# Optimization experiments

Measured on AMD Instinct MI355X. Metric: run time of the kernel, lower is better.

The kernel has to match this reference:

```python
import jax, jax.numpy as jnp
import numpy as np

MARGIN = 0.2  # init kwarg
_EPS = 1e-12


def _pairwise_dist(x):
    # Euclidean cdist via the Gram trick; safe sqrt so grads stay finite at d=0.
    sq = jnp.sum(x * x, axis=1)
    d2 = sq[:, None] + sq[None, :] - 2.0 * (x @ x.T)
    d2 = jnp.maximum(d2, 0.0)
    safe = jnp.where(d2 > _EPS, d2, _EPS)
    return jnp.where(d2 > _EPS, jnp.sqrt(safe), 0.0)


def setup_inputs() -> dict:
    key = jax.random.key(0)
    k1, k2 = jax.random.split(key)
    B, D = 8192, 128
    embeddings = jax.random.normal(k1, (B, D), dtype=jnp.float32)
    labels = jax.random.randint(k2, (B,), 0, 64)
    return {"embeddings": embeddings, "labels": labels}


def reference(embeddings, labels):
    B = embeddings.shape[0]
    d = _pairwise_dist(embeddings)                      # [B, B]
    eq = labels[None, :] == labels[:, None]             # [B, B] bool (incl. diag)
    pos_mask = eq.astype(d.dtype) - jnp.eye(B, dtype=d.dtype)  # positives, no self
    hardest_positive = jnp.max(d * pos_mask, axis=1)    # [B]
    max_dist = jnp.max(d)
    # push non-negatives (same label, incl. self) out of the min
    hardest_negative = jnp.min(d + max_dist * eq.astype(d.dtype), axis=1)  # [B]
    losses = jax.nn.relu(hardest_positive - hardest_negative + MARGIN)
    return jnp.mean(losses)
```

## Files before the change

kernel.cpp:

```cpp
#include <hip/hip_runtime.h>
#include <hip/hip_bf16.h>


#define BB 8192
#define DD 128
#define MARGIN 0.2f
#define EPS 1e-12f

#define COLS_PER_BLOCK 512
#define ROWS_PER_BLOCK 256
#define STAGE_COLS 64
#define NSTAGES 8
#define STAGE_SHORTS (STAGE_COLS * DD)

typedef __attribute__((ext_vector_type(8))) short short8;
typedef __attribute__((ext_vector_type(16))) float f32x16;

__device__ inline unsigned short f2bf(float f) {
    __hip_bfloat16 h = __float2bfloat16(f);
    unsigned short u;
    __builtin_memcpy(&u, &h, 2);
    return u;
}

__global__ __launch_bounds__(256) void prep_kernel(
    const float* __restrict__ x, const int* __restrict__ lab,
    unsigned short* __restrict__ xb, float2* __restrict__ meta,
    unsigned* __restrict__ hp2, unsigned* __restrict__ mn2,
    unsigned long long* __restrict__ fsum, unsigned* __restrict__ fdone) {
    int t = blockIdx.x * blockDim.x + threadIdx.x;
    int row = t >> 5;
    const float4 v = reinterpret_cast<const float4*>(x)[t];

    union { unsigned short u[4]; uint2 w; } p;
    p.u[0] = f2bf(v.x); p.u[1] = f2bf(v.y);
    p.u[2] = f2bf(v.z); p.u[3] = f2bf(v.w);
    reinterpret_cast<uint2*>(xb)[t] = p.w;

    float s = v.x * v.x + v.y * v.y + v.z * v.z + v.w * v.w;
    #pragma unroll
    for (int m = 16; m >= 1; m >>= 1) s += __shfl_xor(s, m, 64);
    if ((t & 31) == 0) meta[row] = make_float2(s, __int_as_float(lab[row]));

    if (t < BB) { hp2[t] = 0u; mn2[t] = 0x7f800000u; }
    if (t == 0) { *fsum = 0ull; *fdone = 0u; }
}

__global__ __launch_bounds__(512) void triplet_main(
    const unsigned short* __restrict__ xb, const float2* __restrict__ meta,
    unsigned* __restrict__ hp2, unsigned* __restrict__ mn2) {
    const int tid  = threadIdx.x;
    const int wave = tid >> 6;
    const int lane = tid & 63;
    const int l31  = lane & 31;
    const int lh1  = lane >> 5;
    const int rbase = blockIdx.x * ROWS_PER_BLOCK + wave * 32;
    const int cbase = blockIdx.y * COLS_PER_BLOCK;

    __shared__ unsigned short sb[3][STAGE_SHORTS];
    __shared__ float2 smeta[COLS_PER_BLOCK];

    short8 a[8];
    {
        const unsigned short* ar = xb + (size_t)(rbase + l31) * DD + lh1 * 8;
        #pragma unroll
        for (int s = 0; s < 8; ++s)
            a[s] = *reinterpret_cast<const short8*>(ar + s * 16);
    }

    unsigned li4[4];
    float hp[16], mn[16];
    #pragma unroll
    for (int q = 0; q < 4; ++q) {
        unsigned w = 0;
        #pragma unroll
        for (int k = 0; k < 4; ++k) {
            const int rl = 8 * q + 4 * lh1 + k;
            w |= ((unsigned)__float_as_int(meta[rbase + rl].y) & 255u) << (8 * k);
        }
        li4[q] = w;
    }
    #pragma unroll
    for (int r = 0; r < 16; ++r) { hp[r] = -__builtin_inff(); mn[r] = __builtin_inff(); }

    smeta[tid] = meta[cbase + tid];

    auto stage = [&](int g, int buf) {
        const char* src_base = (const char*)(xb + (size_t)(cbase + g * STAGE_COLS) * DD);
        #pragma unroll
        for (int p = 0; p < 2; ++p) {
            const int o   = p * 8192 + tid * 16;
            const int row = o >> 8;
            const int byt = (o & 255) ^ ((row & 15) << 4);
            const char* src = src_base + row * 256 + byt;
            char* dst = (char*)&sb[buf][0] + p * 8192 + wave * 1024;
            __builtin_amdgcn_global_load_lds(
                (const __attribute__((address_space(1))) void*)src,
                (__attribute__((address_space(3))) void*)dst, 16, 0, 0);
        }
    };

    auto compute_group = [&](int st, int gg, int buf) {
        const char* base = (const char*)&sb[buf][0];
        const int jl = gg * 32 + l31;
        const int rowoff = jl * 256;
        const int swz = (jl & 15) << 4;
        f32x16 acc = {};
        short8 b[4];
        #pragma unroll
        for (int s = 0; s < 4; ++s)
            b[s] = *reinterpret_cast<const short8*>(
                base + rowoff + ((s * 32 + lh1 * 16) ^ swz));
        #pragma unroll
        for (int s = 0; s < 4; ++s)
            acc = __builtin_amdgcn_mfma_f32_32x32x16_bf16(a[s], b[s], acc, 0, 0, 0);
        #pragma unroll
        for (int s = 0; s < 4; ++s)
            b[s] = *reinterpret_cast<const short8*>(
                base + rowoff + (((s + 4) * 32 + lh1 * 16) ^ swz));
        #pragma unroll
        for (int s = 0; s < 4; ++s)
            acc = __builtin_amdgcn_mfma_f32_32x32x16_bf16(a[s + 4], b[s], acc, 0, 0, 0);

        const float2 mj = smeta[st * STAGE_COLS + jl];
        const float sqj = mj.x;
        const int   lj  = __float_as_int(mj.y);
        #pragma unroll
        for (int q = 0; q < 4; ++q) {
            const unsigned lw = li4[q];
            #pragma unroll
            for (int k = 0; k < 4; ++k) {
                const int r = q * 4 + k;
                const float d2p = fmaf(acc[r], -2.0f, sqj);
                const bool eq = (int)((lw >> (8 * k)) & 255u) == lj;
                hp[r] = fmaxf(hp[r], eq ? d2p : -__builtin_inff());
                mn[r] = fminf(mn[r], eq ? __builtin_inff() : d2p);
            }
        }
    };

    stage(0, 0);
    stage(1, 1);
    #define PIPE_ITER(ST, PEND)                                            \
        asm volatile("s_waitcnt vmcnt(" #PEND ")" ::: "memory");           \
        __syncthreads();                                                   \
        if ((ST) + 2 < NSTAGES) stage((ST) + 2, ((ST) + 2) % 3);           \
        compute_group((ST), 0, (ST) % 3);                                  \
        compute_group((ST), 1, (ST) % 3);
    PIPE_ITER(0, 2)
    PIPE_ITER(1, 2)
    PIPE_ITER(2, 2)
    PIPE_ITER(3, 2)
    PIPE_ITER(4, 2)
    PIPE_ITER(5, 2)
    PIPE_ITER(6, 2)
    PIPE_ITER(7, 0)
    #undef PIPE_ITER

    #pragma unroll
    for (int r = 0; r < 16; ++r) {
        const int rl = (r & 3) + 8 * (r >> 2) + 4 * lh1;
        const float sqi = meta[rbase + rl].x;
        hp[r] = fmaxf(sqi + hp[r], 0.0f);
        mn[r] = sqi + mn[r];
    }
    #pragma unroll
    for (int m = 1; m < 32; m <<= 1) {
        #pragma unroll
        for (int r = 0; r < 16; ++r) {
            hp[r] = fmaxf(hp[r], __shfl_xor(hp[r], m, 64));
            mn[r] = fminf(mn[r], __shfl_xor(mn[r], m, 64));
        }
    }
    if (l31 == 0) {
        #pragma unroll
        for (int r = 0; r < 16; ++r) {
            const int i = rbase + (r & 3) + 8 * (r >> 2) + 4 * lh1;
            atomicMax(&hp2[i], __float_as_uint(hp[r]));
            atomicMin(&mn2[i], __float_as_uint(mn[r]));
        }
    }
}

__device__ inline float d_of(float d2) {
    return (d2 > EPS) ? sqrtf(d2) : 0.0f;
}

__global__ __launch_bounds__(1024) void finalize_kernel(
    const unsigned* __restrict__ hp2, const unsigned* __restrict__ mn2,
    unsigned long long* __restrict__ fsum, unsigned* __restrict__ fdone,
    float* __restrict__ out) {
    const int i = blockIdx.x * 1024 + threadIdx.x;
    const float hpv = d_of(__uint_as_float(hp2[i]));
    const float mnv = d_of(__uint_as_float(mn2[i]));
    float acc = fmaxf(hpv - mnv + MARGIN, 0.0f);

    #pragma unroll
    for (int m = 1; m < 64; m <<= 1) acc += __shfl_xor(acc, m, 64);
    __shared__ float ws[16];
    const int wave = threadIdx.x >> 6;
    if ((threadIdx.x & 63) == 0) ws[wave] = acc;
    __syncthreads();
    if (threadIdx.x == 0) {
        float s = 0.0f;
        #pragma unroll
        for (int w = 0; w < 16; ++w) s += ws[w];
        atomicAdd(fsum, (unsigned long long)((double)s * 4294967296.0));
        __threadfence();
        const unsigned old = atomicAdd(fdone, 1u);
        if (old == gridDim.x - 1) {
            const unsigned long long total = atomicAdd(fsum, 0ull);
            out[0] = (float)((double)total / 4294967296.0 / (double)BB);
        }
    }
}

extern "C" void kernel_launch(void* const* d_in, const int* in_sizes, int n_in,
                              void* d_out, int out_size, void* d_ws, size_t ws_size,
                              hipStream_t stream) {
    const float* x = (const float*)d_in[0];
    const int* lab = (const int*)d_in[1];
    float* out = (float*)d_out;

    char* ws = (char*)d_ws;
    unsigned short* xb = (unsigned short*)ws;
    float2* meta = (float2*)(ws + (size_t)BB * DD * 2);
    unsigned* hp2 = (unsigned*)(ws + (size_t)BB * DD * 2 + BB * 8);
    unsigned* mn2 = (unsigned*)(ws + (size_t)BB * DD * 2 + BB * 12);
    unsigned long long* fsum = (unsigned long long*)(ws + (size_t)BB * DD * 2 + BB * 16);
    unsigned* fdone = (unsigned*)(ws + (size_t)BB * DD * 2 + BB * 16 + 8);

    prep_kernel<<<(BB * DD / 4) / 256, 256, 0, stream>>>(x, lab, xb, meta, hp2, mn2, fsum, fdone);
    dim3 grid(BB / ROWS_PER_BLOCK, BB / COLS_PER_BLOCK);
    triplet_main<<<grid, 512, 0, stream>>>(xb, meta, hp2, mn2);
    finalize_kernel<<<BB / 1024, 1024, 0, stream>>>(hp2, mn2, fsum, fdone, out);
}
```

Measured before the change: 50.18 us.

## Exploit distance symmetry with upper-triangular tiles and fold norms into MFMA

Exploits the symmetry of the distance matrix by launching only upper-triangular 256x256 tile pairs. Each tile updates both its row reductions and, through per-column cross-lane reductions and atomics, the column reductions, which roughly halves the MFMA work. The squared-norm terms are folded into an extra bf16 MFMA so the epilogue works directly on scaled accumulator values. This adds per-group column atomics and shuffles, and it loses precision because the norms pass through bf16. It also swaps __syncthreads for a raw barrier with a scheduling fence.

```diff
diff --git a/kernel.cpp b/kernel.cpp
--- a/kernel.cpp
+++ b/kernel.cpp
@@ -7,10 +7,11 @@
 #define MARGIN 0.2f
 #define EPS 1e-12f
 
-#define COLS_PER_BLOCK 512
-#define ROWS_PER_BLOCK 256
+#define NBLK 32
+#define TILE 256
+#define NTRI (NBLK * (NBLK + 1) / 2)
 #define STAGE_COLS 64
-#define NSTAGES 8
+#define NSTAGES 4
 #define STAGE_SHORTS (STAGE_COLS * DD)
 
 typedef __attribute__((ext_vector_type(8))) short short8;
@@ -54,11 +55,15 @@
     const int lane = tid & 63;
     const int l31  = lane & 31;
     const int lh1  = lane >> 5;
-    const int rbase = blockIdx.x * ROWS_PER_BLOCK + wave * 32;
-    const int cbase = blockIdx.y * COLS_PER_BLOCK;
+
+    int bi = 0, rem = (int)blockIdx.x;
+    while (rem >= NBLK - bi) { rem -= NBLK - bi; ++bi; }
+    const int bj = bi + rem;
+    const int rbase = bi * TILE + wave * 32;
+    const int cbase = bj * TILE;
 
     __shared__ unsigned short sb[3][STAGE_SHORTS];
-    __shared__ float2 smeta[COLS_PER_BLOCK];
+    __shared__ float2 smeta[TILE];
 
     short8 a[8];
     {
@@ -67,9 +72,13 @@
         for (int s = 0; s < 8; ++s)
             a[s] = *reinterpret_cast<const short8*>(ar + s * 16);
     }
+    short8 a9 = {0, 0, 0, 0, 0, 0, 0, 0};
+    if (lh1 == 0) {
+        a9[0] = (short)f2bf(meta[rbase + l31].x);
+        a9[1] = (short)0x3F80;
+    }
 
     unsigned li4[4];
-    float hp[16], mn[16];
     #pragma unroll
     for (int q = 0; q < 4; ++q) {
         unsigned w = 0;
@@ -80,10 +89,11 @@
         }
         li4[q] = w;
     }
-    #pragma unroll
-    for (int r = 0; r < 16; ++r) { hp[r] = -__builtin_inff(); mn[r] = __builtin_inff(); }
-
-    smeta[tid] = meta[cbase + tid];
+    float hpa[16], mna[16];
+    #pragma unroll
+    for (int r = 0; r < 16; ++r) { hpa[r] = __builtin_inff(); mna[r] = -__builtin_inff(); }
+
+    if (tid < TILE) smeta[tid] = meta[cbase + tid];
 
     auto stage = [&](int g, int buf) {
         const char* src_base = (const char*)(xb + (size_t)(cbase + g * STAGE_COLS) * DD);
@@ -105,7 +115,16 @@
         const int jl = gg * 32 + l31;
         const int rowoff = jl * 256;
         const int swz = (jl & 15) << 4;
+        const float2 mj = smeta[st * STAGE_COLS + jl];
+        const int lj = __float_as_int(mj.y) & 255;
+
+        short8 b9 = {0, 0, 0, 0, 0, 0, 0, 0};
+        if (lh1 == 0) {
+            b9[0] = (short)0xBF00;
+            b9[1] = (short)f2bf(-0.5f * mj.x);
+        }
         f32x16 acc = {};
+        acc = __builtin_amdgcn_mfma_f32_32x32x16_bf16(a9, b9, acc, 0, 0, 0);
         short8 b[4];
         #pragma unroll
         for (int s = 0; s < 4; ++s)
@@ -122,62 +141,60 @@
         for (int s = 0; s < 4; ++s)
             acc = __builtin_amdgcn_mfma_f32_32x32x16_bf16(a[s + 4], b[s], acc, 0, 0, 0);
 
-        const float2 mj = smeta[st * STAGE_COLS + jl];
-        const float sqj = mj.x;
-        const int   lj  = __float_as_int(mj.y);
+        float hpc = __builtin_inff(), mnc = -__builtin_inff();
         #pragma unroll
         for (int q = 0; q < 4; ++q) {
             const unsigned lw = li4[q];
             #pragma unroll
             for (int k = 0; k < 4; ++k) {
                 const int r = q * 4 + k;
-                const float d2p = fmaf(acc[r], -2.0f, sqj);
                 const bool eq = (int)((lw >> (8 * k)) & 255u) == lj;
-                hp[r] = fmaxf(hp[r], eq ? d2p : -__builtin_inff());
-                mn[r] = fminf(mn[r], eq ? __builtin_inff() : d2p);
+                const float sp = eq ? acc[r] : __builtin_inff();
+                const float sn = eq ? -__builtin_inff() : acc[r];
+                hpa[r] = fminf(hpa[r], sp);
+                mna[r] = fmaxf(mna[r], sn);
+                hpc = fminf(hpc, sp);
+                mnc = fmaxf(mnc, sn);
             }
+        }
+        hpc = fminf(hpc, __shfl_xor(hpc, 32, 64));
+        mnc = fmaxf(mnc, __shfl_xor(mnc, 32, 64));
+        if (lh1 == 0) {
+            const int j = cbase + st * STAGE_COLS + jl;
+            atomicMax(&hp2[j], __float_as_uint(fmaxf(hpc * -2.0f, 0.0f)));
+            atomicMin(&mn2[j], __float_as_uint(mnc * -2.0f));
         }
     };
 
     stage(0, 0);
     stage(1, 1);
-    #define PIPE_ITER(ST, PEND)                                            \
-        asm volatile("s_waitcnt vmcnt(" #PEND ")" ::: "memory");           \
-        __syncthreads();                                                   \
-        if ((ST) + 2 < NSTAGES) stage((ST) + 2, ((ST) + 2) % 3);           \
-        compute_group((ST), 0, (ST) % 3);                                  \
+    #define PIPE_ITER(ST, PEND)                                                \
+        asm volatile("s_waitcnt lgkmcnt(0) vmcnt(" #PEND ")" ::: "memory");    \
+        __builtin_amdgcn_s_barrier();                                          \
+        __builtin_amdgcn_sched_barrier(0);                                     \
+        if ((ST) + 2 < NSTAGES) stage((ST) + 2, ((ST) + 2) % 3);               \
+        compute_group((ST), 0, (ST) % 3);                                      \
         compute_group((ST), 1, (ST) % 3);
     PIPE_ITER(0, 2)
     PIPE_ITER(1, 2)
     PIPE_ITER(2, 2)
-    PIPE_ITER(3, 2)
-    PIPE_ITER(4, 2)
-    PIPE_ITER(5, 2)
-    PIPE_ITER(6, 2)
-    PIPE_ITER(7, 0)
+    PIPE_ITER(3, 0)
     #undef PIPE_ITER
 
     #pragma unroll
-    for (int r = 0; r < 16; ++r) {
-        const int rl = (r & 3) + 8 * (r >> 2) + 4 * lh1;
-        const float sqi = meta[rbase + rl].x;
-        hp[r] = fmaxf(sqi + hp[r], 0.0f);
-        mn[r] = sqi + mn[r];
-    }
-    #pragma unroll
     for (int m = 1; m < 32; m <<= 1) {
         #pragma unroll
         for (int r = 0; r < 16; ++r) {
-            hp[r] = fmaxf(hp[r], __shfl_xor(hp[r], m, 64));
-            mn[r] = fminf(mn[r], __shfl_xor(mn[r], m, 64));
+            hpa[r] = fminf(hpa[r], __shfl_xor(hpa[r], m, 64));
+            mna[r] = fmaxf(mna[r], __shfl_xor(mna[r], m, 64));
         }
     }
     if (l31 == 0) {
         #pragma unroll
         for (int r = 0; r < 16; ++r) {
             const int i = rbase + (r & 3) + 8 * (r >> 2) + 4 * lh1;
-            atomicMax(&hp2[i], __float_as_uint(hp[r]));
-            atomicMin(&mn2[i], __float_as_uint(mn[r]));
+            atomicMax(&hp2[i], __float_as_uint(fmaxf(hpa[r] * -2.0f, 0.0f)));
+            atomicMin(&mn2[i], __float_as_uint(mna[r] * -2.0f));
         }
     }
 }
@@ -231,7 +248,6 @@
     unsigned* fdone = (unsigned*)(ws + (size_t)BB * DD * 2 + BB * 16 + 8);
 
     prep_kernel<<<(BB * DD / 4) / 256, 256, 0, stream>>>(x, lab, xb, meta, hp2, mn2, fsum, fdone);
-    dim3 grid(BB / ROWS_PER_BLOCK, BB / COLS_PER_BLOCK);
-    triplet_main<<<grid, 512, 0, stream>>>(xb, meta, hp2, mn2);
+    triplet_main<<<NTRI, 512, 0, stream>>>(xb, meta, hp2, mn2);
     finalize_kernel<<<BB / 1024, 1024, 0, stream>>>(hp2, mn2, fsum, fdone, out);
 }
```

New measurement: 86.87 us. 73.1% more time.

## Switch to 16x16x32 MFMA tiles with smaller row blocks and finer pipeline stages

Applied to the files above, without the earlier changes.

Replaces the 32x32x16 bf16 MFMA tiling with 16x16x32 tiles: each wave now owns 16 rows instead of 32, blocks cover 128 rows, and stages hold 32 columns across 16 pipeline steps. This cuts per-thread register state (4 accumulators and mins/maxes instead of 16) and doubles the grid, aiming for more occupancy and better load balance. The pipeline uses explicit s_barrier plus sched_barrier and tighter waitcnt. In exchange, each column tile is reloaded by twice as many blocks, and there are more barriers per column processed.

```diff
diff --git a/kernel.cpp b/kernel.cpp
--- a/kernel.cpp
+++ b/kernel.cpp
@@ -8,13 +8,13 @@
 #define EPS 1e-12f
 
 #define COLS_PER_BLOCK 512
-#define ROWS_PER_BLOCK 256
-#define STAGE_COLS 64
-#define NSTAGES 8
+#define ROWS_PER_BLOCK 128
+#define STAGE_COLS 32
+#define NSTAGES 16
 #define STAGE_SHORTS (STAGE_COLS * DD)
 
 typedef __attribute__((ext_vector_type(8))) short short8;
-typedef __attribute__((ext_vector_type(16))) float f32x16;
+typedef __attribute__((ext_vector_type(4))) float f32x4;
 
 __device__ inline unsigned short f2bf(float f) {
     __hip_bfloat16 h = __float2bfloat16(f);
@@ -52,130 +52,107 @@
     const int tid  = threadIdx.x;
     const int wave = tid >> 6;
     const int lane = tid & 63;
-    const int l31  = lane & 31;
-    const int lh1  = lane >> 5;
-    const int rbase = blockIdx.x * ROWS_PER_BLOCK + wave * 32;
+    const int l15  = lane & 15;
+    const int lhi  = lane >> 4;
+    const int rbase = blockIdx.x * ROWS_PER_BLOCK + wave * 16;
     const int cbase = blockIdx.y * COLS_PER_BLOCK;
 
     __shared__ unsigned short sb[3][STAGE_SHORTS];
     __shared__ float2 smeta[COLS_PER_BLOCK];
 
-    short8 a[8];
+    short8 a[4];
     {
-        const unsigned short* ar = xb + (size_t)(rbase + l31) * DD + lh1 * 8;
-        #pragma unroll
-        for (int s = 0; s < 8; ++s)
-            a[s] = *reinterpret_cast<const short8*>(ar + s * 16);
-    }
-
-    unsigned li4[4];
-    float hp[16], mn[16];
-    #pragma unroll
-    for (int q = 0; q < 4; ++q) {
-        unsigned w = 0;
-        #pragma unroll
-        for (int k = 0; k < 4; ++k) {
-            const int rl = 8 * q + 4 * lh1 + k;
-            w |= ((unsigned)__float_as_int(meta[rbase + rl].y) & 255u) << (8 * k);
-        }
-        li4[q] = w;
-    }
-    #pragma unroll
-    for (int r = 0; r < 16; ++r) { hp[r] = -__builtin_inff(); mn[r] = __builtin_inff(); }
+        const unsigned short* ar = xb + (size_t)(rbase + l15) * DD + lhi * 8;
+        #pragma unroll
+        for (int s = 0; s < 4; ++s)
+            a[s] = *reinterpret_cast<const short8*>(ar + s * 32);
+    }
+
+    unsigned liw = 0;
+    {
+        #pragma unroll
+        for (int k = 0; k < 4; ++k)
+            liw |= ((unsigned)__float_as_int(meta[rbase + lhi * 4 + k].y) & 255u) << (8 * k);
+    }
+    float hp[4], mn[4];
+    #pragma unroll
+    for (int r = 0; r < 4; ++r) { hp[r] = -__builtin_inff(); mn[r] = __builtin_inff(); }
 
     smeta[tid] = meta[cbase + tid];
 
     auto stage = [&](int g, int buf) {
         const char* src_base = (const char*)(xb + (size_t)(cbase + g * STAGE_COLS) * DD);
-        #pragma unroll
-        for (int p = 0; p < 2; ++p) {
-            const int o   = p * 8192 + tid * 16;
-            const int row = o >> 8;
-            const int byt = (o & 255) ^ ((row & 15) << 4);
-            const char* src = src_base + row * 256 + byt;
-            char* dst = (char*)&sb[buf][0] + p * 8192 + wave * 1024;
-            __builtin_amdgcn_global_load_lds(
-                (const __attribute__((address_space(1))) void*)src,
-                (__attribute__((address_space(3))) void*)dst, 16, 0, 0);
-        }
+        const int o   = tid * 16;
+        const int row = o >> 8;
+        const int byt = (o & 255) ^ ((row & 15) << 4);
+        const char* src = src_base + row * 256 + byt;
+        char* dst = (char*)&sb[buf][0] + wave * 1024;
+        __builtin_amdgcn_global_load_lds(
+            (const __attribute__((address_space(1))) void*)src,
+            (__attribute__((address_space(3))) void*)dst, 16, 0, 0);
     };
 
-    auto compute_group = [&](int st, int gg, int buf) {
-        const char* base = (const char*)&sb[buf][0];
-        const int jl = gg * 32 + l31;
+    auto compute_group = [&](int st, int gg, const char* base) {
+        const int jl = gg * 16 + l15;
         const int rowoff = jl * 256;
         const int swz = (jl & 15) << 4;
-        f32x16 acc = {};
         short8 b[4];
         #pragma unroll
         for (int s = 0; s < 4; ++s)
             b[s] = *reinterpret_cast<const short8*>(
-                base + rowoff + ((s * 32 + lh1 * 16) ^ swz));
+                base + rowoff + ((s * 64 + lhi * 16) ^ swz));
+        f32x4 acc = {};
         #pragma unroll
         for (int s = 0; s < 4; ++s)
-            acc = __builtin_amdgcn_mfma_f32_32x32x16_bf16(a[s], b[s], acc, 0, 0, 0);
-        #pragma unroll
-        for (int s = 0; s < 4; ++s)
-            b[s] = *reinterpret_cast<const short8*>(
-                base + rowoff + (((s + 4) * 32 + lh1 * 16) ^ swz));
-        #pragma unroll
-        for (int s = 0; s < 4; ++s)
-            acc = __builtin_amdgcn_mfma_f32_32x32x16_bf16(a[s + 4], b[s], acc, 0, 0, 0);
+            acc = __builtin_amdgcn_mfma_f32_16x16x32_bf16(a[s], b[s], acc, 0, 0, 0);
 
         const float2 mj = smeta[st * STAGE_COLS + jl];
         const float sqj = mj.x;
-        const int   lj  = __float_as_int(mj.y);
-        #pragma unroll
-        for (int q = 0; q < 4; ++q) {
-            const unsigned lw = li4[q];
-            #pragma unroll
-            for (int k = 0; k < 4; ++k) {
-                const int r = q * 4 + k;
-                const float d2p = fmaf(acc[r], -2.0f, sqj);
-                const bool eq = (int)((lw >> (8 * k)) & 255u) == lj;
-                hp[r] = fmaxf(hp[r], eq ? d2p : -__builtin_inff());
-                mn[r] = fminf(mn[r], eq ? __builtin_inff() : d2p);
-            }
+        const int   lj  = __float_as_int(mj.y) & 255;
+        #pragma unroll
+        for (int r = 0; r < 4; ++r) {
+            const float d2p = fmaf(acc[r], -2.0f, sqj);
+            const bool eq = (int)((liw >> (8 * r)) & 255u) == lj;
+            hp[r] = fmaxf(hp[r], eq ? d2p : -__builtin_inff());
+            mn[r] = fminf(mn[r], eq ? __builtin_inff() : d2p);
         }
     };
 
     stage(0, 0);
     stage(1, 1);
-    #define PIPE_ITER(ST, PEND)                                            \
-        asm volatile("s_waitcnt vmcnt(" #PEND ")" ::: "memory");           \
-        __syncthreads();                                                   \
-        if ((ST) + 2 < NSTAGES) stage((ST) + 2, ((ST) + 2) % 3);           \
-        compute_group((ST), 0, (ST) % 3);                                  \
-        compute_group((ST), 1, (ST) % 3);
-    PIPE_ITER(0, 2)
-    PIPE_ITER(1, 2)
-    PIPE_ITER(2, 2)
-    PIPE_ITER(3, 2)
-    PIPE_ITER(4, 2)
-    PIPE_ITER(5, 2)
-    PIPE_ITER(6, 2)
-    PIPE_ITER(7, 0)
-    #undef PIPE_ITER
-
-    #pragma unroll
-    for (int r = 0; r < 16; ++r) {
-        const int rl = (r & 3) + 8 * (r >> 2) + 4 * lh1;
-        const float sqi = meta[rbase + rl].x;
+    #pragma unroll
+    for (int st = 0; st < NSTAGES; ++st) {
+        if (st < NSTAGES - 1)
+            asm volatile("s_waitcnt lgkmcnt(0) vmcnt(1)" ::: "memory");
+        else
+            asm volatile("s_waitcnt lgkmcnt(0) vmcnt(0)" ::: "memory");
+        __builtin_amdgcn_s_barrier();
+        __builtin_amdgcn_sched_barrier(0);
+        if (st + 2 < NSTAGES) stage(st + 2, (st + 2) % 3);
+        const char* base = (const char*)&sb[st % 3][0];
+        compute_group(st, 0, base);
+        __builtin_amdgcn_sched_barrier(0);
+        compute_group(st, 1, base);
+    }
+
+    #pragma unroll
+    for (int r = 0; r < 4; ++r) {
+        const float sqi = meta[rbase + lhi * 4 + r].x;
         hp[r] = fmaxf(sqi + hp[r], 0.0f);
         mn[r] = sqi + mn[r];
     }
     #pragma unroll
-    for (int m = 1; m < 32; m <<= 1) {
-        #pragma unroll
-        for (int r = 0; r < 16; ++r) {
+    for (int m = 1; m < 16; m <<= 1) {
+        #pragma unroll
+        for (int r = 0; r < 4; ++r) {
             hp[r] = fmaxf(hp[r], __shfl_xor(hp[r], m, 64));
             mn[r] = fminf(mn[r], __shfl_xor(mn[r], m, 64));
         }
     }
-    if (l31 == 0) {
-        #pragma unroll
-        for (int r = 0; r < 16; ++r) {
-            const int i = rbase + (r & 3) + 8 * (r >> 2) + 4 * lh1;
+    if (l15 == 0) {
+        #pragma unroll
+        for (int r = 0; r < 4; ++r) {
+            const int i = rbase + lhi * 4 + r;
             atomicMax(&hp2[i], __float_as_uint(hp[r]));
             atomicMin(&mn2[i], __float_as_uint(mn[r]));
         }
```

Result: faster. 40.16 us (-20.0%).
